# Kernel optimization log

Measured on AMD Instinct MI355X. Metric: run time of the kernel, lower is better.

The kernel has to match this reference:

```python
import jax, jax.numpy as jnp
import numpy as np

M, B, E, A = 3, 65536, 512, 256  # modalities, batch, embedding_dim, attention_dim
LN_EPS = 1e-5


def setup_inputs() -> dict:
    key = jax.random.key(0)
    ks = jax.random.split(key, 9)
    s_e = 1.0 / np.sqrt(E)
    s_a = 1.0 / np.sqrt(A)
    return {
        "x": jax.random.normal(ks[0], (M, B, E), jnp.float32),
        "Wq": jax.random.normal(ks[1], (M, E, A), jnp.float32) * s_e,
        "bq": jax.random.normal(ks[2], (M, A), jnp.float32) * s_e,
        "Wk": jax.random.normal(ks[3], (M, E, A), jnp.float32) * s_e,
        "bk": jax.random.normal(ks[4], (M, A), jnp.float32) * s_e,
        "v": jax.random.normal(ks[5], (M, A), jnp.float32) * s_a,
        "Wt": jax.random.normal(ks[6], (M, M, E, E), jnp.float32) * s_e,
        "bt": jax.random.normal(ks[7], (M, M, E), jnp.float32) * s_e,
        "gamma": jnp.ones((M * E,), jnp.float32),
        "beta": jnp.zeros((M * E,), jnp.float32),
    }


def reference(x, Wq, bq, Wk, bk, v, Wt, bt, gamma, beta):
    # Per-modality query/key projections (batched over modality axis m).
    qp = jnp.einsum('mbe,mea->mba', x, Wq) + bq[:, None, :]  # [M,B,A]
    kp = jnp.einsum('mbe,mea->mba', x, Wk) + bk[:, None, :]  # [M,B,A]
    # Additive score: v_q^T tanh(q_proj[q] + k_proj[k]) for every (q,k) pair.
    t = jnp.tanh(qp[:, None, :, :] + kp[None, :, :, :])       # [Q,K,B,A]
    scores = jnp.einsum('qa,qkba->qkb', v, t)                  # [Q,K,B]
    # Exclude k == q from the softmax (torch code skips key_mod == query_mod).
    diag = jnp.eye(scores.shape[0], dtype=bool)[:, :, None]
    scores = jnp.where(diag, -jnp.inf, scores)
    alpha = jax.nn.softmax(scores, axis=1)                     # [Q,K,B], zero on diag
    # Weighted sum of per-pair linear transforms of the key embeddings.
    att = (jnp.einsum('qkb,kbe,qkef->qbf', alpha, x, Wt)
           + jnp.einsum('qkb,qke->qbe', alpha, bt))            # [Q,B,E]
    attended = x + att                                         # residual per modality
    # Concat modalities along features, then LayerNorm over M*E.
    fused = jnp.transpose(attended, (1, 0, 2)).reshape(x.shape[1], -1)  # [B, M*E]
    mu = jnp.mean(fused, axis=-1, keepdims=True)
    var = jnp.var(fused, axis=-1, keepdims=True)
    fused = (fused - mu) * jax.lax.rsqrt(var + LN_EPS) * gamma + beta
    return fused
```

## Files before the change

kernel.cpp:

```cpp
#include <hip/hip_runtime.h>
#include <hip/hip_bf16.h>

#define MOD   3
#define BATCH 65536
#define EDIM  512
#define ADIM  256
#define FEAT  1536

typedef __attribute__((ext_vector_type(8))) short   s16x8;
typedef __attribute__((ext_vector_type(8))) __bf16  bf16x8;
typedef __attribute__((ext_vector_type(4))) float   f32x4;
typedef __attribute__((ext_vector_type(4))) unsigned short u16x4;

__device__ __forceinline__ float b2f(unsigned short u) {
    union { unsigned int ui; float f; } c; c.ui = ((unsigned int)u) << 16; return c.f;
}
__device__ __forceinline__ unsigned short f2b(float f) {
    __hip_bfloat16 h = __float2bfloat16(f);
    return __builtin_bit_cast(unsigned short, h);
}

__device__ __forceinline__ void glds16(const unsigned short* g, unsigned short* l) {
    __builtin_amdgcn_global_load_lds(
        (const __attribute__((address_space(1))) void*)g,
        (__attribute__((address_space(3))) void*)l, 16, 0, 0);
}

#define WAITV(N) asm volatile("s_waitcnt vmcnt(%0)" :: "i"(N) : "memory")
__device__ __forceinline__ void BAR() {
    asm volatile("" ::: "memory");
    __builtin_amdgcn_s_barrier();
    asm volatile("" ::: "memory");
}

__global__ __launch_bounds__(256) void k_convert_x(const float* __restrict__ x,
                                                   unsigned short* __restrict__ xb, int n4) {
    int i = blockIdx.x * blockDim.x + threadIdx.x;
    int stride = gridDim.x * blockDim.x;
    for (; i < n4; i += stride) {
        f32x4 v = *((const f32x4*)x + i);
        u16x4 o;
        for (int j = 0; j < 4; ++j) o[j] = f2b(v[j]);
        *((u16x4*)xb + i) = o;
    }
}

__global__ __launch_bounds__(256) void k_prep_w(const float* __restrict__ Wq,
                                                const float* __restrict__ Wk,
                                                const float* __restrict__ Wt,
                                                unsigned short* __restrict__ wqk,
                                                unsigned short* __restrict__ wtt3) {
    int i = blockIdx.x * blockDim.x + threadIdx.x;
    int stride = gridDim.x * blockDim.x;
    for (int idx = i; idx < MOD * EDIM * EDIM; idx += stride) {
        int m = idx / (EDIM * EDIM); int r = idx % (EDIM * EDIM);
        int n = r / EDIM; int e = r % EDIM;
        float f = (n < ADIM) ? Wq[(m * EDIM + e) * ADIM + n]
                             : Wk[(m * EDIM + e) * ADIM + (n - ADIM)];
        wqk[idx] = f2b(f);
    }
    for (int idx = i; idx < MOD * 1024 * EDIM; idx += stride) {
        int q = idx / (1024 * EDIM); int r = idx % (1024 * EDIM);
        int n = r / EDIM; int e = r % EDIM;
        int kp = n >> 9, f = n & 511;
        int k = (q + 1 + kp) % 3;
        wtt3[idx] = f2b(Wt[((size_t)(q * 3 + k) * EDIM + e) * EDIM + f]);
    }
}


struct GCtx {
    const unsigned short* pA[2];
    const unsigned short* pB[2];
    const unsigned short* lds;
    unsigned short* ldsW;
    int aoff, boff;
};

__device__ __forceinline__ void gctx_init(GCtx& c,
                                          const unsigned short* Ag0, const unsigned short* Ag1,
                                          const unsigned short* Bg0, const unsigned short* Bg1,
                                          unsigned short* lds) {
    const int tid = threadIdx.x, lane = tid & 63, wid = tid >> 6;
    const int wm = wid >> 2, wn = wid & 3;
    int stageRow = wid * 32 + (lane >> 2);
    int gsrc8 = ((lane & 3) ^ ((lane >> 3) & 3)) * 8;
    size_t so = (size_t)stageRow * 512 + gsrc8;
    c.pA[0] = Ag0 + so; c.pA[1] = Ag1 + so;
    c.pB[0] = Bg0 + so; c.pB[1] = Bg1 + so;
    c.lds = lds;
    c.ldsW = lds + wid * 1024;
    int swz8 = ((lane >> 4) ^ ((lane >> 1) & 3)) * 8;
    c.aoff = (wm * 128 + (lane & 15)) * 32 + swz8;
    c.boff = (wn * 64 + (lane & 15)) * 32 + swz8;
}

template<int NU>
__device__ __forceinline__ void stage_s(const GCtx& c, int s) {
    if (s >= NU) return;
    int p = s >> 5;
    int sp = s & 31;
    int colK = (sp >> 2) * 64 + (sp & 2) * 16;
    const unsigned short* src = ((sp & 1) ? c.pB[p] : c.pA[p]) + colK;
    unsigned short* dst = c.ldsW + (s & 7) * 8192;
    glds16(src, dst);
    glds16(src + 16 * 512, dst + 512);
}

template<int Q>
__device__ __forceinline__ void phase_compute(int T, const GCtx& c,
                                              s16x8 (&bfr)[4], f32x4 (&acc)[8][4]) {
    constexpr int ks = Q >> 1, rh = Q & 1;
    const unsigned short* Asl = c.lds + ((T & 1) * 4 + 2 * ks) * 8192;
    const unsigned short* Bsl = Asl + 8192;
    s16x8 af[4];
#pragma unroll
    for (int i = 0; i < 4; ++i) af[i] = *(const s16x8*)(Asl + c.aoff + (rh * 4 + i) * 512);
    if constexpr ((Q & 1) == 0) {
#pragma unroll
        for (int j = 0; j < 4; ++j) bfr[j] = *(const s16x8*)(Bsl + c.boff + j * 512);
    }
    __builtin_amdgcn_s_setprio(1);
#pragma unroll
    for (int i = 0; i < 4; ++i)
#pragma unroll
        for (int j = 0; j < 4; ++j)
            acc[rh * 4 + i][j] = __builtin_amdgcn_mfma_f32_16x16x32_bf16(
                __builtin_bit_cast(bf16x8, af[i]), __builtin_bit_cast(bf16x8, bfr[j]),
                acc[rh * 4 + i][j], 0, 0, 0);
    __builtin_amdgcn_s_setprio(0);
}

template<int W0, int W2, int NU>
__device__ __forceinline__ void do_tile(int T, const GCtx& c,
                                        s16x8 (&bfr)[4], f32x4 (&acc)[8][4]) {
    stage_s<NU>(c, 4 * T + 6);
    WAITV(W0); BAR();
    phase_compute<0>(T, c, bfr, acc);
    BAR();
    stage_s<NU>(c, 4 * T + 7);
    phase_compute<1>(T, c, bfr, acc);
    BAR();
    stage_s<NU>(c, 4 * T + 8);
    WAITV(W2); BAR();
    phase_compute<2>(T, c, bfr, acc);
    BAR();
    stage_s<NU>(c, 4 * T + 9);
    phase_compute<3>(T, c, bfr, acc);
    BAR();
}

__global__ __launch_bounds__(512, 2) void k_gemm_proj(const unsigned short* __restrict__ xb,
                                                      const unsigned short* __restrict__ wqk,
                                                      const float* __restrict__ bq,
                                                      const float* __restrict__ bk,
                                                      unsigned short* __restrict__ proj) {
    __shared__ __align__(16) unsigned short LDS[65536];
    int l = (blockIdx.x & 7) * 192 + (blockIdx.x >> 3);
    int ct = l & 1, rt = (l >> 1) & 255, m = l >> 9;
    int row0 = rt * 256, col0 = ct * 256;
    f32x4 acc[8][4];
#pragma unroll
    for (int i = 0; i < 8; ++i) for (int j = 0; j < 4; ++j) acc[i][j] = (f32x4)0.f;
    GCtx c;
    const unsigned short* Ag = xb + ((size_t)m * BATCH + row0) * EDIM;
    const unsigned short* Bg = wqk + ((size_t)m * EDIM + col0) * EDIM;
    gctx_init(c, Ag, Ag, Bg, Bg, LDS);
    s16x8 bfr[4];
#pragma unroll
    for (int s = 0; s < 6; ++s) stage_s<32>(c, s);
#pragma unroll 1
    for (int t = 0; t < 6; ++t) do_tile<10, 10, 32>(t, c, bfr, acc);
    do_tile<10, 8, 32>(6, c, bfr, acc);
    do_tile<4, 0, 32>(7, c, bfr, acc);
    int lane = threadIdx.x & 63, wid = threadIdx.x >> 6;
    int wm = wid >> 2, wn = wid & 3;
#pragma unroll
    for (int j = 0; j < 4; ++j) {
        int col = col0 + wn * 64 + j * 16 + (lane & 15);
        float bias = (col < ADIM) ? bq[m * ADIM + col] : bk[m * ADIM + col - ADIM];
#pragma unroll
        for (int i8 = 0; i8 < 8; ++i8) {
            int rbase = row0 + wm * 128 + i8 * 16 + (lane >> 4) * 4;
#pragma unroll
            for (int r = 0; r < 4; ++r)
                proj[((size_t)m * BATCH + rbase + r) * EDIM + col] = f2b(acc[i8][j][r] + bias);
        }
    }
}

__global__ __launch_bounds__(256) void k_scores(const unsigned short* __restrict__ proj,
                                                const float* __restrict__ v,
                                                float* __restrict__ alpha) {
    int wid = threadIdx.x >> 6, lane = threadIdx.x & 63;
    size_t b = (size_t)blockIdx.x * 4 + wid;
    float qp[3][4], kp[3][4], vq[3][4];
    for (int m = 0; m < 3; ++m) {
        const unsigned short* p = proj + ((size_t)m * BATCH + b) * EDIM;
        u16x4 uq = *(const u16x4*)(p + lane * 4);
        u16x4 uk = *(const u16x4*)(p + ADIM + lane * 4);
        f32x4 vv = *((const f32x4*)(v + m * ADIM) + lane);
        for (int j = 0; j < 4; ++j) { qp[m][j] = b2f(uq[j]); kp[m][j] = b2f(uk[j]); vq[m][j] = vv[j]; }
    }
    for (int q = 0; q < 3; ++q) {
        float s[2];
        for (int ki = 0; ki < 2; ++ki) {
            int k = (q + 1 + ki) % 3;
            float a = 0.f;
            for (int j = 0; j < 4; ++j) a += vq[q][j] * tanhf(qp[q][j] + kp[k][j]);
            for (int off = 32; off; off >>= 1) a += __shfl_xor(a, off, 64);
            s[ki] = a;
        }
        if (lane == 0) {
            float mx = fmaxf(s[0], s[1]);
            float e0 = expf(s[0] - mx), e1 = expf(s[1] - mx);
            float inv = 1.f / (e0 + e1);
            alpha[(size_t)(q * 2 + 0) * BATCH + b] = e0 * inv;
            alpha[(size_t)(q * 2 + 1) * BATCH + b] = e1 * inv;
        }
    }
}

__global__ __launch_bounds__(512, 2) void k_gemm_att(const unsigned short* __restrict__ xb,
                                                     const unsigned short* __restrict__ wtt3,
                                                     const float* __restrict__ alpha,
                                                     const float* __restrict__ bt,
                                                     unsigned short* __restrict__ att) {
    __shared__ __align__(16) unsigned short LDS[65536];
    __shared__ float auxA0[256], auxA1[256], auxR[256];
    int l = (blockIdx.x & 7) * 192 + (blockIdx.x >> 3);
    int ct = l & 1, rt = (l >> 1) & 255, q = l >> 9;
    int row0 = rt * 256, col0 = ct * 256;
    int kA = (q + 1) % 3, kB = (q + 2) % 3;
    int tid = threadIdx.x, lane = tid & 63, wid = tid >> 6;
    int wm = wid >> 2, wn = wid & 3;

    if (tid < 256) {
        float a0 = alpha[(size_t)(q * 2 + 0) * BATCH + row0 + tid];
        float a1 = alpha[(size_t)(q * 2 + 1) * BATCH + row0 + tid];
        auxA0[tid] = a0; auxA1[tid] = a1;
        auxR[tid] = a0 / fmaxf(a1, 1e-30f);
    }
    __syncthreads();

    f32x4 acc[8][4];
#pragma unroll
    for (int i = 0; i < 8; ++i) for (int j = 0; j < 4; ++j) acc[i][j] = (f32x4)0.f;
    GCtx c;
    gctx_init(c,
              xb + ((size_t)kA * BATCH + row0) * EDIM,
              xb + ((size_t)kB * BATCH + row0) * EDIM,
              wtt3 + ((size_t)(q * 2 + 0) * EDIM + col0) * EDIM,
              wtt3 + ((size_t)(q * 2 + 1) * EDIM + col0) * EDIM,
              LDS);
    s16x8 bfr[4];
#pragma unroll
    for (int s = 0; s < 6; ++s) stage_s<64>(c, s);
#pragma unroll 1
    for (int t = 0; t < 8; ++t) do_tile<10, 10, 64>(t, c, bfr, acc);
#pragma unroll
    for (int i8 = 0; i8 < 8; ++i8) {
        int rl = wm * 128 + i8 * 16 + (lane >> 4) * 4;
        f32x4 rv = *(const f32x4*)&auxR[rl];
#pragma unroll
        for (int j = 0; j < 4; ++j)
#pragma unroll
            for (int r = 0; r < 4; ++r) acc[i8][j][r] *= rv[r];
    }
#pragma unroll 1
    for (int t = 8; t < 14; ++t) do_tile<10, 10, 64>(t, c, bfr, acc);
    do_tile<10, 8, 64>(14, c, bfr, acc);
    do_tile<4, 0, 64>(15, c, bfr, acc);

    float btAv[4], btBv[4];
#pragma unroll
    for (int j = 0; j < 4; ++j) {
        int col = col0 + wn * 64 + j * 16 + (lane & 15);
        btAv[j] = bt[(size_t)(q * 3 + kA) * EDIM + col];
        btBv[j] = bt[(size_t)(q * 3 + kB) * EDIM + col];
    }
#pragma unroll
    for (int i8 = 0; i8 < 8; ++i8) {
        int rl = wm * 128 + i8 * 16 + (lane >> 4) * 4;
        f32x4 a0v = *(const f32x4*)&auxA0[rl];
        f32x4 a1v = *(const f32x4*)&auxA1[rl];
        int rbase = row0 + rl;
#pragma unroll
        for (int j = 0; j < 4; ++j) {
            int col = col0 + wn * 64 + j * 16 + (lane & 15);
#pragma unroll
            for (int r = 0; r < 4; ++r)
                att[((size_t)q * BATCH + rbase + r) * EDIM + col] =
                    f2b(a1v[r] * acc[i8][j][r] + a0v[r] * btAv[j] + a1v[r] * btBv[j]);
        }
    }
}

__global__ __launch_bounds__(192) void k_fuse_ln(const unsigned short* __restrict__ xb,
                                                 const unsigned short* __restrict__ att,
                                                 const float* __restrict__ gamma,
                                                 const float* __restrict__ beta,
                                                 float* __restrict__ out) {
    __shared__ float red[2][3];
    int b = blockIdx.x, t = threadIdx.x, m = t >> 6, lane = t & 63;
    int e0 = lane * 8;
    s16x8 xv = *(const s16x8*)(xb + ((size_t)m * BATCH + b) * EDIM + e0);
    s16x8 av = *(const s16x8*)(att + ((size_t)m * BATCH + b) * EDIM + e0);
    float v[8]; float s = 0.f, s2 = 0.f;
#pragma unroll
    for (int j = 0; j < 8; ++j) {
        float vv = b2f((unsigned short)xv[j]) + b2f((unsigned short)av[j]);
        v[j] = vv; s += vv; s2 += vv * vv;
    }
    for (int off = 32; off; off >>= 1) { s += __shfl_xor(s, off, 64); s2 += __shfl_xor(s2, off, 64); }
    if (lane == 0) { red[0][m] = s; red[1][m] = s2; }
    __syncthreads();
    float S = red[0][0] + red[0][1] + red[0][2];
    float S2 = red[1][0] + red[1][1] + red[1][2];
    float mu  = S * (1.f / 1536.f);
    float var = S2 * (1.f / 1536.f) - mu * mu;
    float rs  = rsqrtf(var + 1e-5f);
    int f0 = m * EDIM + e0;
    f32x4 g0 = *(const f32x4*)(gamma + f0), g1 = *(const f32x4*)(gamma + f0 + 4);
    f32x4 be0 = *(const f32x4*)(beta + f0), be1 = *(const f32x4*)(beta + f0 + 4);
    f32x4 o0, o1;
#pragma unroll
    for (int j = 0; j < 4; ++j) {
        o0[j] = (v[j]     - mu) * rs * g0[j] + be0[j];
        o1[j] = (v[j + 4] - mu) * rs * g1[j] + be1[j];
    }
    float* op = out + (size_t)b * FEAT + f0;
    *(f32x4*)op = o0; *(f32x4*)(op + 4) = o1;
}

extern "C" void kernel_launch(void* const* d_in, const int* in_sizes, int n_in,
                              void* d_out, int out_size, void* d_ws, size_t ws_size,
                              hipStream_t stream) {
    const float* x     = (const float*)d_in[0];
    const float* Wq    = (const float*)d_in[1];
    const float* bq    = (const float*)d_in[2];
    const float* Wk    = (const float*)d_in[3];
    const float* bk    = (const float*)d_in[4];
    const float* v     = (const float*)d_in[5];
    const float* Wt    = (const float*)d_in[6];
    const float* bt    = (const float*)d_in[7];
    const float* gamma = (const float*)d_in[8];
    const float* beta  = (const float*)d_in[9];
    float* out = (float*)d_out;

    char* ws = (char*)d_ws;
    unsigned short* wqk   = (unsigned short*)(ws);
    unsigned short* wtt3  = (unsigned short*)(ws + 1572864);
    float*          alpha = (float*)        (ws + 4718592);
    unsigned short* xb    = (unsigned short*)(ws + 6291456);
    unsigned short* att   = (unsigned short*)(ws + 207618048);
    unsigned short* proj  = att;

    k_convert_x<<<4096, 256, 0, stream>>>(x, xb, (MOD * BATCH * EDIM) / 4);
    k_prep_w   <<<2048, 256, 0, stream>>>(Wq, Wk, Wt, wqk, wtt3);
    k_gemm_proj<<<1536, 512, 0, stream>>>(xb, wqk, bq, bk, proj);
    k_scores   <<<16384, 256, 0, stream>>>(proj, v, alpha);
    k_gemm_att <<<1536, 512, 0, stream>>>(xb, wtt3, alpha, bt, att);
    k_fuse_ln  <<<65536, 192, 0, stream>>>(xb, att, gamma, beta, out);
}
```

Measured before the change: 751.1 us.

## Restructure GEMM main loop into separate LDS-load and MFMA phases with sched barriers

Splits each compute phase into a pre-phase and an MFMA phase. The pre-phase reads A/B fragments from LDS and issues the next global-to-LDS stage; the MFMA phase runs the matrix multiplies. Sched barriers stop the compiler from interleaving the two, and the vmcnt waits move to the end of each 2-phase pair so the wait for the next slab sits after the current fragments are loaded. The goal is cleaner overlap of memory traffic with MFMA work and fewer stalls at barriers. Changing the wait counts and the pipeline offsets risks LDS read/write hazards if the staging distance is off.

```diff
diff --git a/kernel.cpp b/kernel.cpp
--- a/kernel.cpp
+++ b/kernel.cpp
@@ -27,6 +27,7 @@
 }
 
 #define WAITV(N) asm volatile("s_waitcnt vmcnt(%0)" :: "i"(N) : "memory")
+#define SCHED0() __builtin_amdgcn_sched_barrier(0)
 __device__ __forceinline__ void BAR() {
     asm volatile("" ::: "memory");
     __builtin_amdgcn_s_barrier();
@@ -107,19 +108,25 @@
     glds16(src + 16 * 512, dst + 512);
 }
 
-template<int Q>
-__device__ __forceinline__ void phase_compute(int T, const GCtx& c,
-                                              s16x8 (&bfr)[4], f32x4 (&acc)[8][4]) {
+template<int NU, int Q>
+__device__ __forceinline__ void pre_phase(const GCtx& c, int T,
+                                          s16x8 (&af)[4], s16x8 (&bfr)[4]) {
     constexpr int ks = Q >> 1, rh = Q & 1;
     const unsigned short* Asl = c.lds + ((T & 1) * 4 + 2 * ks) * 8192;
     const unsigned short* Bsl = Asl + 8192;
-    s16x8 af[4];
 #pragma unroll
     for (int i = 0; i < 4; ++i) af[i] = *(const s16x8*)(Asl + c.aoff + (rh * 4 + i) * 512);
-    if constexpr ((Q & 1) == 0) {
+    if constexpr (rh == 0) {
 #pragma unroll
         for (int j = 0; j < 4; ++j) bfr[j] = *(const s16x8*)(Bsl + c.boff + j * 512);
     }
+    stage_s<NU>(c, 4 * T + 6 + Q);
+}
+
+template<int Q>
+__device__ __forceinline__ void mfma_phase(s16x8 (&af)[4], s16x8 (&bfr)[4],
+                                           f32x4 (&acc)[8][4]) {
+    constexpr int rh = Q & 1;
     __builtin_amdgcn_s_setprio(1);
 #pragma unroll
     for (int i = 0; i < 4; ++i)
@@ -131,23 +138,31 @@
     __builtin_amdgcn_s_setprio(0);
 }
 
-template<int W0, int W2, int NU>
+template<int W1, int W3, int NU>
 __device__ __forceinline__ void do_tile(int T, const GCtx& c,
-                                        s16x8 (&bfr)[4], f32x4 (&acc)[8][4]) {
-    stage_s<NU>(c, 4 * T + 6);
-    WAITV(W0); BAR();
-    phase_compute<0>(T, c, bfr, acc);
-    BAR();
-    stage_s<NU>(c, 4 * T + 7);
-    phase_compute<1>(T, c, bfr, acc);
-    BAR();
-    stage_s<NU>(c, 4 * T + 8);
-    WAITV(W2); BAR();
-    phase_compute<2>(T, c, bfr, acc);
-    BAR();
-    stage_s<NU>(c, 4 * T + 9);
-    phase_compute<3>(T, c, bfr, acc);
-    BAR();
+                                        s16x8 (&af)[4], s16x8 (&bfr)[4],
+                                        f32x4 (&acc)[8][4]) {
+    pre_phase<NU, 0>(c, T, af, bfr);
+    BAR(); SCHED0();
+    mfma_phase<0>(af, bfr, acc);
+    SCHED0(); BAR();
+
+    pre_phase<NU, 1>(c, T, af, bfr);
+    WAITV(W1);
+    BAR(); SCHED0();
+    mfma_phase<1>(af, bfr, acc);
+    SCHED0(); BAR();
+
+    pre_phase<NU, 2>(c, T, af, bfr);
+    BAR(); SCHED0();
+    mfma_phase<2>(af, bfr, acc);
+    SCHED0(); BAR();
+
+    pre_phase<NU, 3>(c, T, af, bfr);
+    WAITV(W3);
+    BAR(); SCHED0();
+    mfma_phase<3>(af, bfr, acc);
+    SCHED0(); BAR();
 }
 
 __global__ __launch_bounds__(512, 2) void k_gemm_proj(const unsigned short* __restrict__ xb,
@@ -166,13 +181,15 @@
     const unsigned short* Ag = xb + ((size_t)m * BATCH + row0) * EDIM;
     const unsigned short* Bg = wqk + ((size_t)m * EDIM + col0) * EDIM;
     gctx_init(c, Ag, Ag, Bg, Bg, LDS);
-    s16x8 bfr[4];
+    s16x8 af[4], bfr[4];
 #pragma unroll
     for (int s = 0; s < 6; ++s) stage_s<32>(c, s);
+    WAITV(8);
+    BAR();
 #pragma unroll 1
-    for (int t = 0; t < 6; ++t) do_tile<10, 10, 32>(t, c, bfr, acc);
-    do_tile<10, 8, 32>(6, c, bfr, acc);
-    do_tile<4, 0, 32>(7, c, bfr, acc);
+    for (int t = 0; t < 6; ++t) do_tile<8, 8, 32>(t, c, af, bfr, acc);
+    do_tile<8, 4, 32>(6, c, af, bfr, acc);
+    do_tile<0, 0, 32>(7, c, af, bfr, acc);
     int lane = threadIdx.x & 63, wid = threadIdx.x >> 6;
     int wm = wid >> 2, wn = wid & 3;
 #pragma unroll
@@ -253,11 +270,13 @@
               wtt3 + ((size_t)(q * 2 + 0) * EDIM + col0) * EDIM,
               wtt3 + ((size_t)(q * 2 + 1) * EDIM + col0) * EDIM,
               LDS);
-    s16x8 bfr[4];
+    s16x8 af[4], bfr[4];
 #pragma unroll
     for (int s = 0; s < 6; ++s) stage_s<64>(c, s);
+    WAITV(8);
+    BAR();
 #pragma unroll 1
-    for (int t = 0; t < 8; ++t) do_tile<10, 10, 64>(t, c, bfr, acc);
+    for (int t = 0; t < 8; ++t) do_tile<8, 8, 64>(t, c, af, bfr, acc);
 #pragma unroll
     for (int i8 = 0; i8 < 8; ++i8) {
         int rl = wm * 128 + i8 * 16 + (lane >> 4) * 4;
@@ -268,9 +287,9 @@
             for (int r = 0; r < 4; ++r) acc[i8][j][r] *= rv[r];
     }
 #pragma unroll 1
-    for (int t = 8; t < 14; ++t) do_tile<10, 10, 64>(t, c, bfr, acc);
-    do_tile<10, 8, 64>(14, c, bfr, acc);
-    do_tile<4, 0, 64>(15, c, bfr, acc);
+    for (int t = 8; t < 14; ++t) do_tile<8, 8, 64>(t, c, af, bfr, acc);
+    do_tile<8, 4, 64>(14, c, af, bfr, acc);
+    do_tile<0, 0, 64>(15, c, af, bfr, acc);
 
     float btAv[4], btBv[4];
 #pragma unroll
```

Result: no change. 751.2 us (+0.0%).

## Software-pipeline LDS fragment reads one phase ahead of MFMA compute in GEMMs

Applied to the files above, without the earlier changes.

Restructures both GEMM main loops so each phase window loads the next phase's A/B fragments from LDS into double-buffered registers before issuing the current phase's MFMAs. The global-to-LDS stage for the next sub-step is issued inside the same window with retuned vmcnt waits. It also cuts barriers to one per window. The aim is to hide LDS read latency behind matrix-core work and reduce barrier stalls, at the cost of more fragment registers, which could pressure occupancy at 2 waves/SIMD, plus a more fragile wait-count schedule.

```diff
diff --git a/kernel.cpp b/kernel.cpp
--- a/kernel.cpp
+++ b/kernel.cpp
@@ -107,47 +107,73 @@
     glds16(src + 16 * 512, dst + 512);
 }
 
-template<int Q>
-__device__ __forceinline__ void phase_compute(int T, const GCtx& c,
-                                              s16x8 (&bfr)[4], f32x4 (&acc)[8][4]) {
-    constexpr int ks = Q >> 1, rh = Q & 1;
-    const unsigned short* Asl = c.lds + ((T & 1) * 4 + 2 * ks) * 8192;
-    const unsigned short* Bsl = Asl + 8192;
-    s16x8 af[4];
-#pragma unroll
-    for (int i = 0; i < 4; ++i) af[i] = *(const s16x8*)(Asl + c.aoff + (rh * 4 + i) * 512);
-    if constexpr ((Q & 1) == 0) {
-#pragma unroll
-        for (int j = 0; j < 4; ++j) bfr[j] = *(const s16x8*)(Bsl + c.boff + j * 512);
-    }
+template<int Q, int W, int NU, bool DOREAD>
+__device__ __forceinline__ void window_f(int T, const GCtx& c,
+                                         s16x8 (&af0)[4], s16x8 (&af1)[4],
+                                         s16x8 (&bf0)[4], s16x8 (&bf1)[4],
+                                         f32x4 (&acc)[8][4]) {
+    BAR();
+    if constexpr (DOREAD) {
+        constexpr int Qn = (Q + 1) & 3;
+        constexpr int ksn = Qn >> 1, rhn = Qn & 1;
+        int Tn = (Q == 3) ? (T + 1) : T;
+        const unsigned short* Asl = c.lds + ((Tn & 1) * 4 + 2 * ksn) * 8192;
+        const unsigned short* Bsl = Asl + 8192;
+#pragma unroll
+        for (int i = 0; i < 4; ++i) {
+            s16x8 v = *(const s16x8*)(Asl + c.aoff + (rhn * 4 + i) * 512);
+            if constexpr ((Qn & 1) == 0) af0[i] = v; else af1[i] = v;
+        }
+        if constexpr (Qn == 0) {
+#pragma unroll
+            for (int j = 0; j < 4; ++j) bf0[j] = *(const s16x8*)(Bsl + c.boff + j * 512);
+        }
+        if constexpr (Qn == 2) {
+#pragma unroll
+            for (int j = 0; j < 4; ++j) bf1[j] = *(const s16x8*)(Bsl + c.boff + j * 512);
+        }
+    }
+    stage_s<NU>(c, 4 * T + Q + 6);
+    WAITV(W);
     __builtin_amdgcn_s_setprio(1);
+    constexpr int RH = Q & 1;
 #pragma unroll
     for (int i = 0; i < 4; ++i)
 #pragma unroll
-        for (int j = 0; j < 4; ++j)
-            acc[rh * 4 + i][j] = __builtin_amdgcn_mfma_f32_16x16x32_bf16(
-                __builtin_bit_cast(bf16x8, af[i]), __builtin_bit_cast(bf16x8, bfr[j]),
-                acc[rh * 4 + i][j], 0, 0, 0);
+        for (int j = 0; j < 4; ++j) {
+            const s16x8& a = (Q & 1) ? af1[i] : af0[i];
+            const s16x8& b = (Q >> 1) ? bf1[j] : bf0[j];
+            acc[RH * 4 + i][j] = __builtin_amdgcn_mfma_f32_16x16x32_bf16(
+                __builtin_bit_cast(bf16x8, a), __builtin_bit_cast(bf16x8, b),
+                acc[RH * 4 + i][j], 0, 0, 0);
+        }
     __builtin_amdgcn_s_setprio(0);
 }
 
-template<int W0, int W2, int NU>
-__device__ __forceinline__ void do_tile(int T, const GCtx& c,
-                                        s16x8 (&bfr)[4], f32x4 (&acc)[8][4]) {
-    stage_s<NU>(c, 4 * T + 6);
-    WAITV(W0); BAR();
-    phase_compute<0>(T, c, bfr, acc);
+template<int W0, int W1, int W2, int W3, int NU, bool LASTT>
+__device__ __forceinline__ void do_tile2(int T, const GCtx& c,
+                                         s16x8 (&af0)[4], s16x8 (&af1)[4],
+                                         s16x8 (&bf0)[4], s16x8 (&bf1)[4],
+                                         f32x4 (&acc)[8][4]) {
+    window_f<0, W0, NU, true  >(T, c, af0, af1, bf0, bf1, acc);
+    window_f<1, W1, NU, true  >(T, c, af0, af1, bf0, bf1, acc);
+    window_f<2, W2, NU, true  >(T, c, af0, af1, bf0, bf1, acc);
+    window_f<3, W3, NU, !LASTT>(T, c, af0, af1, bf0, bf1, acc);
+}
+
+template<int NU>
+__device__ __forceinline__ void pipe_prologue(const GCtx& c,
+                                              s16x8 (&af0)[4], s16x8 (&bf0)[4]) {
+#pragma unroll
+    for (int s = 0; s < 6; ++s) stage_s<NU>(c, s);
+    WAITV(8);
     BAR();
-    stage_s<NU>(c, 4 * T + 7);
-    phase_compute<1>(T, c, bfr, acc);
-    BAR();
-    stage_s<NU>(c, 4 * T + 8);
-    WAITV(W2); BAR();
-    phase_compute<2>(T, c, bfr, acc);
-    BAR();
-    stage_s<NU>(c, 4 * T + 9);
-    phase_compute<3>(T, c, bfr, acc);
-    BAR();
+    const unsigned short* Asl = c.lds;
+    const unsigned short* Bsl = c.lds + 8192;
+#pragma unroll
+    for (int i = 0; i < 4; ++i) af0[i] = *(const s16x8*)(Asl + c.aoff + i * 512);
+#pragma unroll
+    for (int j = 0; j < 4; ++j) bf0[j] = *(const s16x8*)(Bsl + c.boff + j * 512);
 }
 
 __global__ __launch_bounds__(512, 2) void k_gemm_proj(const unsigned short* __restrict__ xb,
@@ -166,13 +192,12 @@
     const unsigned short* Ag = xb + ((size_t)m * BATCH + row0) * EDIM;
     const unsigned short* Bg = wqk + ((size_t)m * EDIM + col0) * EDIM;
     gctx_init(c, Ag, Ag, Bg, Bg, LDS);
-    s16x8 bfr[4];
-#pragma unroll
-    for (int s = 0; s < 6; ++s) stage_s<32>(c, s);
+    s16x8 af0[4], af1[4], bf0[4], bf1[4];
+    pipe_prologue<32>(c, af0, bf0);
 #pragma unroll 1
-    for (int t = 0; t < 6; ++t) do_tile<10, 10, 32>(t, c, bfr, acc);
-    do_tile<10, 8, 32>(6, c, bfr, acc);
-    do_tile<4, 0, 32>(7, c, bfr, acc);
+    for (int t = 0; t < 6; ++t) do_tile2<6, 6, 6, 6, 32, false>(t, c, af0, af1, bf0, bf1, acc);
+    do_tile2<6, 6, 4, 2, 32, false>(6, c, af0, af1, bf0, bf1, acc);
+    do_tile2<0, 0, 0, 0, 32, true >(7, c, af0, af1, bf0, bf1, acc);
     int lane = threadIdx.x & 63, wid = threadIdx.x >> 6;
     int wm = wid >> 2, wn = wid & 3;
 #pragma unroll
@@ -253,11 +278,10 @@
               wtt3 + ((size_t)(q * 2 + 0) * EDIM + col0) * EDIM,
               wtt3 + ((size_t)(q * 2 + 1) * EDIM + col0) * EDIM,
               LDS);
-    s16x8 bfr[4];
-#pragma unroll
-    for (int s = 0; s < 6; ++s) stage_s<64>(c, s);
+    s16x8 af0[4], af1[4], bf0[4], bf1[4];
+    pipe_prologue<64>(c, af0, bf0);
 #pragma unroll 1
-    for (int t = 0; t < 8; ++t) do_tile<10, 10, 64>(t, c, bfr, acc);
+    for (int t = 0; t < 8; ++t) do_tile2<6, 6, 6, 6, 64, false>(t, c, af0, af1, bf0, bf1, acc);
 #pragma unroll
     for (int i8 = 0; i8 < 8; ++i8) {
         int rl = wm * 128 + i8 * 16 + (lane >> 4) * 4;
@@ -268,9 +292,9 @@
             for (int r = 0; r < 4; ++r) acc[i8][j][r] *= rv[r];
     }
 #pragma unroll 1
-    for (int t = 8; t < 14; ++t) do_tile<10, 10, 64>(t, c, bfr, acc);
-    do_tile<10, 8, 64>(14, c, bfr, acc);
-    do_tile<4, 0, 64>(15, c, bfr, acc);
+    for (int t = 8; t < 14; ++t) do_tile2<6, 6, 6, 6, 64, false>(t, c, af0, af1, bf0, bf1, acc);
+    do_tile2<6, 6, 4, 2, 64, false>(14, c, af0, af1, bf0, bf1, acc);
+    do_tile2<0, 0, 0, 0, 64, true >(15, c, af0, af1, bf0, bf1, acc);
 
     float btAv[4], btBv[4];
 #pragma unroll
```

Result: no change. 747.9 us (median of 2 runs) (-0.4%).

## Restructure GEMM main loop into two-phase windows with earlier LDS fragment loads

Applied to the files above, without the earlier changes.

Replaces the four-phase per-tile schedule with two windows per tile. Each window loads all A and B fragments from LDS first, then issues the next two global-to-LDS stages, waits, and runs 32 MFMAs. The prologue now prefetches four stages instead of six, and the ring slot indexing changes from (T&1)*4+2*ks to u0&7. This is meant to cut the number of barriers and waits per tile and let the MFMA block overlap the in-flight global loads. In exchange it holds more fragment registers and keeps a shallower prefetch depth, so latency hiding and occupancy could suffer.

```diff
diff --git a/kernel.cpp b/kernel.cpp
--- a/kernel.cpp
+++ b/kernel.cpp
@@ -107,46 +107,37 @@
     glds16(src + 16 * 512, dst + 512);
 }
 
-template<int Q>
-__device__ __forceinline__ void phase_compute(int T, const GCtx& c,
-                                              s16x8 (&bfr)[4], f32x4 (&acc)[8][4]) {
-    constexpr int ks = Q >> 1, rh = Q & 1;
-    const unsigned short* Asl = c.lds + ((T & 1) * 4 + 2 * ks) * 8192;
-    const unsigned short* Bsl = Asl + 8192;
-    s16x8 af[4];
-#pragma unroll
-    for (int i = 0; i < 4; ++i) af[i] = *(const s16x8*)(Asl + c.aoff + (rh * 4 + i) * 512);
-    if constexpr ((Q & 1) == 0) {
-#pragma unroll
-        for (int j = 0; j < 4; ++j) bfr[j] = *(const s16x8*)(Bsl + c.boff + j * 512);
-    }
+template<int W, int NU>
+__device__ __forceinline__ void window2(int T, int ks, const GCtx& c, f32x4 (&acc)[8][4]) {
+    int u0 = 4 * T + 2 * ks;
+    const unsigned short* Asl = c.lds + (size_t)(u0 & 7) * 8192;
+    const unsigned short* Bsl = c.lds + (size_t)((u0 + 1) & 7) * 8192;
+    s16x8 af[8], bf[4];
+#pragma unroll
+    for (int j = 0; j < 4; ++j) bf[j] = *(const s16x8*)(Bsl + c.boff + j * 512);
+#pragma unroll
+    for (int i = 0; i < 8; ++i) af[i] = *(const s16x8*)(Asl + c.aoff + i * 512);
+    stage_s<NU>(c, u0 + 4);
+    stage_s<NU>(c, u0 + 5);
+    WAITV(W);
+    BAR();
     __builtin_amdgcn_s_setprio(1);
 #pragma unroll
-    for (int i = 0; i < 4; ++i)
+    for (int i = 0; i < 8; ++i)
 #pragma unroll
         for (int j = 0; j < 4; ++j)
-            acc[rh * 4 + i][j] = __builtin_amdgcn_mfma_f32_16x16x32_bf16(
-                __builtin_bit_cast(bf16x8, af[i]), __builtin_bit_cast(bf16x8, bfr[j]),
-                acc[rh * 4 + i][j], 0, 0, 0);
+            acc[i][j] = __builtin_amdgcn_mfma_f32_16x16x32_bf16(
+                __builtin_bit_cast(bf16x8, af[i]), __builtin_bit_cast(bf16x8, bf[j]),
+                acc[i][j], 0, 0, 0);
     __builtin_amdgcn_s_setprio(0);
-}
-
-template<int W0, int W2, int NU>
-__device__ __forceinline__ void do_tile(int T, const GCtx& c,
-                                        s16x8 (&bfr)[4], f32x4 (&acc)[8][4]) {
-    stage_s<NU>(c, 4 * T + 6);
-    WAITV(W0); BAR();
-    phase_compute<0>(T, c, bfr, acc);
     BAR();
-    stage_s<NU>(c, 4 * T + 7);
-    phase_compute<1>(T, c, bfr, acc);
-    BAR();
-    stage_s<NU>(c, 4 * T + 8);
-    WAITV(W2); BAR();
-    phase_compute<2>(T, c, bfr, acc);
-    BAR();
-    stage_s<NU>(c, 4 * T + 9);
-    phase_compute<3>(T, c, bfr, acc);
+}
+
+template<int NU>
+__device__ __forceinline__ void pipe_prologue2(const GCtx& c) {
+#pragma unroll
+    for (int s = 0; s < 4; ++s) stage_s<NU>(c, s);
+    WAITV(4);
     BAR();
 }
 
@@ -166,13 +157,14 @@
     const unsigned short* Ag = xb + ((size_t)m * BATCH + row0) * EDIM;
     const unsigned short* Bg = wqk + ((size_t)m * EDIM + col0) * EDIM;
     gctx_init(c, Ag, Ag, Bg, Bg, LDS);
-    s16x8 bfr[4];
-#pragma unroll
-    for (int s = 0; s < 6; ++s) stage_s<32>(c, s);
+    pipe_prologue2<32>(c);
 #pragma unroll 1
-    for (int t = 0; t < 6; ++t) do_tile<10, 10, 32>(t, c, bfr, acc);
-    do_tile<10, 8, 32>(6, c, bfr, acc);
-    do_tile<4, 0, 32>(7, c, bfr, acc);
+    for (int t = 0; t < 7; ++t) {
+        window2<4, 32>(t, 0, c, acc);
+        window2<4, 32>(t, 1, c, acc);
+    }
+    window2<0, 32>(7, 0, c, acc);
+    window2<0, 32>(7, 1, c, acc);
     int lane = threadIdx.x & 63, wid = threadIdx.x >> 6;
     int wm = wid >> 2, wn = wid & 3;
 #pragma unroll
@@ -253,11 +245,12 @@
               wtt3 + ((size_t)(q * 2 + 0) * EDIM + col0) * EDIM,
               wtt3 + ((size_t)(q * 2 + 1) * EDIM + col0) * EDIM,
               LDS);
-    s16x8 bfr[4];
-#pragma unroll
-    for (int s = 0; s < 6; ++s) stage_s<64>(c, s);
+    pipe_prologue2<64>(c);
 #pragma unroll 1
-    for (int t = 0; t < 8; ++t) do_tile<10, 10, 64>(t, c, bfr, acc);
+    for (int t = 0; t < 8; ++t) {
+        window2<4, 64>(t, 0, c, acc);
+        window2<4, 64>(t, 1, c, acc);
+    }
 #pragma unroll
     for (int i8 = 0; i8 < 8; ++i8) {
         int rl = wm * 128 + i8 * 16 + (lane >> 4) * 4;
@@ -268,9 +261,12 @@
             for (int r = 0; r < 4; ++r) acc[i8][j][r] *= rv[r];
     }
 #pragma unroll 1
-    for (int t = 8; t < 14; ++t) do_tile<10, 10, 64>(t, c, bfr, acc);
-    do_tile<10, 8, 64>(14, c, bfr, acc);
-    do_tile<4, 0, 64>(15, c, bfr, acc);
+    for (int t = 8; t < 15; ++t) {
+        window2<4, 64>(t, 0, c, acc);
+        window2<4, 64>(t, 1, c, acc);
+    }
+    window2<0, 64>(15, 0, c, acc);
+    window2<0, 64>(15, 1, c, acc);
 
     float btAv[4], btBv[4];
 #pragma unroll
```

Result: slower. 777.0 us (+3.4%).
